# Kernel optimization log

Hardware: AMD Instinct MI355X
Metric: run time of the kernel (lower is better)

Reference implementation:

```python
import jax, jax.numpy as jnp
import numpy as np

B, S, D, H = 2, 2048, 1024, 16
HD = D // H  # 64


def setup_inputs() -> dict:
    key = jax.random.key(0)
    ks = jax.random.split(key, 5)
    sc = 1.0 / np.sqrt(D)
    return {
        "x": jax.random.normal(ks[0], (B, S, D), jnp.float32),
        "wq": jax.random.normal(ks[1], (D, D), jnp.float32) * sc,
        "bq": jnp.zeros((D,), jnp.float32),
        "wk": jax.random.normal(ks[2], (D, D), jnp.float32) * sc,
        "bk": jnp.zeros((D,), jnp.float32),
        "wv": jax.random.normal(ks[3], (D, D), jnp.float32) * sc,
        "bv": jnp.zeros((D,), jnp.float32),
        "wo": jax.random.normal(ks[4], (D, D), jnp.float32) * sc,
        "bo": jnp.zeros((D,), jnp.float32),
    }


def _rope_tables(seq_len, dim):
    inv_freq = 1.0 / (10000.0 ** (jnp.arange(0, dim, 2, dtype=jnp.float32) / dim))
    t = jnp.arange(seq_len, dtype=jnp.float32)
    freqs = jnp.einsum("i,j->ij", t, inv_freq)  # [S, dim/2]
    emb = jnp.concatenate([freqs, freqs], axis=-1)  # [S, dim]
    return jnp.cos(emb)[None, None], jnp.sin(emb)[None, None]  # [1,1,S,dim]


def _rotate_half(x):
    x1, x2 = x[..., : x.shape[-1] // 2], x[..., x.shape[-1] // 2 :]
    return jnp.concatenate([-x2, x1], axis=-1)


def reference(x, wq, bq, wk, bk, wv, bv, wo, bo):
    b, s, d = x.shape
    h, hd = H, d // H
    # projections (torch Linear: x @ W.T + b) -> [b, h, s, hd]
    def proj(w, bias):
        return (x @ w.T + bias).reshape(b, s, h, hd).transpose(0, 2, 1, 3)

    q, k, v = proj(wq, bq), proj(wk, bk), proj(wv, bv)
    cos, sin = _rope_tables(s, hd)
    q = q * cos + _rotate_half(q) * sin
    k = k * cos + _rotate_half(k) * sin
    scores = jnp.einsum("bhqd,bhkd->bhqk", q, k) / jnp.sqrt(jnp.float32(hd))
    attn = jax.nn.softmax(scores, axis=-1)
    out = jnp.einsum("bhqk,bhkd->bhqd", attn, v)
    out = out.transpose(0, 2, 1, 3).reshape(b, s, d)
    return out @ wo.T + bo
```

## Files before the change

kernel.cpp:

```cpp
#include <hip/hip_runtime.h>
#include <hip/hip_bf16.h>

#define Bq 2
#define Sq 2048
#define Dq 1024
#define Hq 16
#define QSCALE 0.18033688011112042f

typedef __attribute__((ext_vector_type(8))) short short8;
typedef __attribute__((ext_vector_type(4))) float floatx4;
typedef unsigned short ushort_t;

#define VMCNT0() asm volatile("s_waitcnt vmcnt(0)" ::: "memory")
#define GLDS(src, dst) __builtin_amdgcn_global_load_lds( \
    (const __attribute__((address_space(1))) void*)(src), \
    (__attribute__((address_space(3))) void*)(dst), 16, 0, 0)

__device__ __forceinline__ ushort_t f2bf(float f) {
    union { float f; unsigned u; } v; v.f = f;
    unsigned u = v.u;
    u += 0x7fffu + ((u >> 16) & 1u);
    return (ushort_t)(u >> 16);
}

__device__ __forceinline__ unsigned pk_bf16(float a, float b) {
    union { __hip_bfloat162 h; unsigned u; } c;
    c.h = __float22bfloat162_rn(float2{a, b});
    return c.u;
}

__device__ __forceinline__ void cvt8(const float* __restrict__ in, ushort_t* __restrict__ out, int i) {
    const float4* p = (const float4*)in + (size_t)i * 2;
    float4 a = p[0], b = p[1];
    ushort4 lo, hi;
    lo.x = f2bf(a.x); lo.y = f2bf(a.y); lo.z = f2bf(a.z); lo.w = f2bf(a.w);
    hi.x = f2bf(b.x); hi.y = f2bf(b.y); hi.z = f2bf(b.z); hi.w = f2bf(b.w);
    *(ushort4*)(out + (size_t)i * 8)     = lo;
    *(ushort4*)(out + (size_t)i * 8 + 4) = hi;
}

__global__ void prep(const float* __restrict__ x,
                     const float* __restrict__ wq, const float* __restrict__ wk,
                     const float* __restrict__ wv, const float* __restrict__ wo,
                     ushort_t* __restrict__ xb,
                     ushort_t* __restrict__ wqb, ushort_t* __restrict__ wkb,
                     ushort_t* __restrict__ wvb, ushort_t* __restrict__ wob,
                     float* __restrict__ cost, float* __restrict__ sint) {
    int b = blockIdx.x;
    if (b < 2048) {
        cvt8(x, xb, b * 256 + threadIdx.x);
    } else if (b < 4096) {
        int w = (b - 2048) >> 9;
        int i = ((b - 2048) & 511) * 256 + threadIdx.x;
        const float* src = (w == 0) ? wq : (w == 1) ? wk : (w == 2) ? wv : wo;
        ushort_t* dst    = (w == 0) ? wqb : (w == 1) ? wkb : (w == 2) ? wvb : wob;
        cvt8(src, dst, i);
    } else {
        int i = (b - 4096) * 256 + threadIdx.x;
        int s = i >> 5, f = i & 31;
        float invf = powf(10000.0f, -(float)f / 32.0f);
        float ang = (float)s * invf;
        cost[i] = cosf(ang);
        sint[i] = sinf(ang);
    }
}

__global__ __launch_bounds__(256, 3) void gemm_qkv(
    const ushort_t* __restrict__ xb,
    const ushort_t* __restrict__ wqb, const ushort_t* __restrict__ wkb, const ushort_t* __restrict__ wvb,
    const float* __restrict__ bq, const float* __restrict__ bk, const float* __restrict__ bv,
    const float* __restrict__ cost, const float* __restrict__ sint,
    ushort_t* __restrict__ qout, ushort_t* __restrict__ kout, ushort_t* __restrict__ vtout)
{
    __shared__ ushort_t As0[128 * 32], As1[128 * 32];
    __shared__ ushort_t Bs0[128 * 32], Bs1[128 * 32];
    const int mode = blockIdx.z;
    const ushort_t* W  = (mode == 0) ? wqb : (mode == 1) ? wkb : wvb;
    const float* bias  = (mode == 0) ? bq  : (mode == 1) ? bk  : bv;

    const int t = threadIdx.x;
    const int lane = t & 63;
    const int wid = t >> 6;
    const int l15 = lane & 15, lk = lane >> 4;
    const int wr = wid >> 1, wc = wid & 1;
    const int rowBase = blockIdx.y * 128;
    const int colBase = blockIdx.x * 128;

    floatx4 acc[4][4] = {};

    const char* aSrc[2];
    const char* bSrc[2];
    int ldso[2];
#pragma unroll
    for (int issue = 0; issue < 2; ++issue) {
        int ldsoff = issue * 4096 + t * 16;
        int row = ldsoff >> 6;
        int cb  = ldsoff & 63;
        ldso[issue] = ldsoff;
        aSrc[issue] = (const char*)xb + (size_t)(rowBase + row) * 2048 + cb;
        bSrc[issue] = (const char*)W  + (size_t)(colBase + row) * 2048 + cb;
    }

    auto STAGE = [&](ushort_t* Ad, ushort_t* Bd) {
#pragma unroll
        for (int issue = 0; issue < 2; ++issue) {
            GLDS(aSrc[issue], (char*)Ad + ldso[issue]);
            GLDS(bSrc[issue], (char*)Bd + ldso[issue]);
        }
        aSrc[0] += 64; aSrc[1] += 64; bSrc[0] += 64; bSrc[1] += 64;
    };

    auto KSTEP = [&](const ushort_t* Ac, const ushort_t* Bc, int knext, ushort_t* An, ushort_t* Bn) {
        if (knext < Dq) STAGE(An, Bn);
        short8 a[4], b[4];
#pragma unroll
        for (int m = 0; m < 4; ++m)
            a[m] = *(const short8*)((const char*)Ac + (wr * 64 + m * 16 + l15) * 64 + lk * 16);
#pragma unroll
        for (int n = 0; n < 4; ++n)
            b[n] = *(const short8*)((const char*)Bc + (wc * 64 + n * 16 + l15) * 64 + lk * 16);
        __builtin_amdgcn_s_setprio(1);
#pragma unroll
        for (int m = 0; m < 4; ++m)
#pragma unroll
            for (int n = 0; n < 4; ++n)
                acc[m][n] = __builtin_amdgcn_mfma_f32_16x16x32_bf16(a[m], b[n], acc[m][n], 0, 0, 0);
        __builtin_amdgcn_s_setprio(0);
        VMCNT0();
        __syncthreads();
    };

    STAGE(As0, Bs0);
    VMCNT0();
    __syncthreads();

#pragma unroll 1
    for (int k0 = 0; k0 < Dq; k0 += 64) {
        KSTEP(As0, Bs0, k0 + 32, As1, Bs1);
        KSTEP(As1, Bs1, k0 + 64, As0, Bs0);
    }

    const int colW = colBase + wc * 64;
    const int hh = colW >> 6;

    if (mode < 2) {
        ushort_t* outp = (mode == 0) ? qout : kout;
        const float osc = (mode == 0) ? QSCALE : 1.0f;
#pragma unroll
        for (int m = 0; m < 4; ++m) {
            int rg0 = rowBase + wr * 64 + m * 16 + lk * 4;
#pragma unroll
            for (int n2 = 0; n2 < 2; ++n2) {
                int d0 = n2 * 16 + l15;
                float b0 = bias[colW + d0];
                float b2 = bias[colW + d0 + 32];
#pragma unroll
                for (int r = 0; r < 4; ++r) {
                    int rg = rg0 + r;
                    int bb = rg >> 11;
                    int s  = rg & 2047;
                    float c  = cost[s * 32 + d0];
                    float sn = sint[s * 32 + d0];
                    float a0 = acc[m][n2][r]     + b0;
                    float a2 = acc[m][n2 + 2][r] + b2;
                    float o0 = (a0 * c - a2 * sn) * osc;
                    float o2 = (a2 * c + a0 * sn) * osc;
                    size_t base = ((size_t)(bb * Hq + hh) * Sq + s) * 64;
                    outp[base + d0]      = f2bf(o0);
                    outp[base + d0 + 32] = f2bf(o2);
                }
            }
        }
    } else {
#pragma unroll
        for (int m = 0; m < 4; ++m) {
            int rg0 = rowBase + wr * 64 + m * 16 + lk * 4;
            int bb  = rg0 >> 11;
            int s0  = rg0 & 2047;
            int g   = (s0 & 63) >> 2;
            int ng  = (g >> 3) * 8 + (g & 3) * 2 + ((g >> 2) & 1);
            int s2b = (s0 & ~63) + ng * 4;
#pragma unroll
            for (int n = 0; n < 4; ++n) {
                int d = n * 16 + l15;
                float bb_ = bias[colW + d];
#pragma unroll
                for (int r = 0; r < 4; ++r)
                    vtout[((size_t)(bb * Hq + hh) * 64 + d) * Sq + s2b + r] = f2bf(acc[m][n][r] + bb_);
            }
        }
    }
}

__global__ __launch_bounds__(256, 3) void flash_attn(
    const ushort_t* __restrict__ qbuf, const ushort_t* __restrict__ kbuf,
    const ushort_t* __restrict__ vtbuf, ushort_t* __restrict__ abuf)
{
    __shared__ char Ks0[64 * 128], Ks1[64 * 128];
    __shared__ char Vs0[64 * 128], Vs1[64 * 128];

    const int t = threadIdx.x, lane = t & 63, wid = t >> 6;
    const int l15 = lane & 15, lk = lane >> 4;

    int flat = blockIdx.y * 16 + blockIdx.x;
    flat = (flat & 7) * 64 + (flat >> 3);
    const int qtile = flat & 15, bh = flat >> 4;
    const int bpos = bh >> 4, h = bh & 15;
    const int qbase = qtile * 128 + wid * 32;

    const ushort_t* Qp = qbuf + ((size_t)bh * Sq + qbase) * 64;
    short8 qf[2][2];
#pragma unroll
    for (int mq = 0; mq < 2; ++mq)
#pragma unroll
        for (int kk = 0; kk < 2; ++kk)
            qf[mq][kk] = *(const short8*)(Qp + (mq * 16 + l15) * 64 + kk * 32 + lk * 8);

    short8 onesf;
#pragma unroll
    for (int j = 0; j < 8; ++j) onesf[j] = (short)0x3F80;

    floatx4 oacc[2][4] = {};
    floatx4 lacc[2] = {};

    int off_[4][2];
#pragma unroll
    for (int n = 0; n < 4; ++n) {
        int swz = (l15 & 7) << 4;
#pragma unroll
        for (int kk = 0; kk < 2; ++kk)
            off_[n][kk] = (n * 16 + l15) * 128 + ((kk * 64 + lk * 16) ^ swz);
    }

    const char* Kg = (const char*)kbuf  + (size_t)bh * Sq * 128;
    const char* Vg = (const char*)vtbuf + (size_t)bh * 64 * Sq * 2;
    unsigned kOff[2], vOff[2];
    int ldso[2];
#pragma unroll
    for (int issue = 0; issue < 2; ++issue) {
        int ldsoff = issue * 4096 + t * 16;
        int row = ldsoff >> 7;
        int pb  = ldsoff & 127;
        int lb  = pb ^ ((row & 7) << 4);
        ldso[issue] = ldsoff;
        kOff[issue] = (unsigned)(row * 128 + lb);
        vOff[issue] = (unsigned)(row * 4096 + lb);
    }

    auto STAGE = [&](char* Kd, char* Vd) {
#pragma unroll
        for (int issue = 0; issue < 2; ++issue) {
            GLDS(Kg + kOff[issue], Kd + ldso[issue]);
            GLDS(Vg + vOff[issue], Vd + ldso[issue]);
        }
        kOff[0] += 8192; kOff[1] += 8192; vOff[0] += 128; vOff[1] += 128;
    };

    auto TILE = [&](const char* Kc, const char* Vc, bool doStage, char* Kn, char* Vn) {
        if (doStage) STAGE(Kn, Vn);

        short8 kf[4][2];
#pragma unroll
        for (int n = 0; n < 4; ++n)
#pragma unroll
            for (int kk = 0; kk < 2; ++kk)
                kf[n][kk] = *(const short8*)(Kc + off_[n][kk]);

        floatx4 sacc[2][4] = {};
        __builtin_amdgcn_s_setprio(1);
#pragma unroll
        for (int kk = 0; kk < 2; ++kk)
#pragma unroll
            for (int n = 0; n < 4; ++n)
#pragma unroll
                for (int mq = 0; mq < 2; ++mq)
                    sacc[mq][n] = __builtin_amdgcn_mfma_f32_16x16x32_bf16(kf[n][kk], qf[mq][kk], sacc[mq][n], 0, 0, 0);
        __builtin_amdgcn_s_setprio(0);

        short8 vf[4][2];
#pragma unroll
        for (int n = 0; n < 4; ++n)
#pragma unroll
            for (int kb = 0; kb < 2; ++kb)
                vf[n][kb] = *(const short8*)(Vc + off_[n][kb]);

        short8 paf[2][2];
#pragma unroll
        for (int mq = 0; mq < 2; ++mq) {
            float p[4][4];
#pragma unroll
            for (int n = 0; n < 4; ++n)
#pragma unroll
                for (int r = 0; r < 4; ++r)
                    p[n][r] = __builtin_exp2f(sacc[mq][n][r]);
#pragma unroll
            for (int kb = 0; kb < 2; ++kb) {
                union { unsigned u[4]; short8 v; } pu;
                pu.u[0] = pk_bf16(p[2 * kb][0],     p[2 * kb][1]);
                pu.u[1] = pk_bf16(p[2 * kb][2],     p[2 * kb][3]);
                pu.u[2] = pk_bf16(p[2 * kb + 1][0], p[2 * kb + 1][1]);
                pu.u[3] = pk_bf16(p[2 * kb + 1][2], p[2 * kb + 1][3]);
                paf[mq][kb] = pu.v;
            }
        }

        __builtin_amdgcn_s_setprio(1);
#pragma unroll
        for (int kb = 0; kb < 2; ++kb) {
#pragma unroll
            for (int n = 0; n < 4; ++n)
#pragma unroll
                for (int mq = 0; mq < 2; ++mq)
                    oacc[mq][n] = __builtin_amdgcn_mfma_f32_16x16x32_bf16(paf[mq][kb], vf[n][kb], oacc[mq][n], 0, 0, 0);
#pragma unroll
            for (int mq = 0; mq < 2; ++mq)
                lacc[mq] = __builtin_amdgcn_mfma_f32_16x16x32_bf16(paf[mq][kb], onesf, lacc[mq], 0, 0, 0);
        }
        __builtin_amdgcn_s_setprio(0);

        VMCNT0();
        __syncthreads();
    };

    STAGE(Ks0, Vs0);
    VMCNT0();
    __syncthreads();

#pragma unroll 1
    for (int i = 0; i < 15; ++i) {
        TILE(Ks0, Vs0, true, Ks1, Vs1);
        TILE(Ks1, Vs1, true, Ks0, Vs0);
    }
    TILE(Ks0, Vs0, true,  Ks1, Vs1);
    TILE(Ks1, Vs1, false, Ks0, Vs0);

#pragma unroll
    for (int mq = 0; mq < 2; ++mq)
#pragma unroll
        for (int r = 0; r < 4; ++r) {
            float linv = 1.0f / lacc[mq][r];
            int srow = qbase + mq * 16 + lk * 4 + r;
            size_t base = ((size_t)bpos * Sq + srow) * Dq + h * 64;
#pragma unroll
            for (int n = 0; n < 4; ++n)
                abuf[base + n * 16 + l15] = f2bf(oacc[mq][n][r] * linv);
        }
}

__global__ __launch_bounds__(256, 4) void gemm_out(
    const ushort_t* __restrict__ ab, const ushort_t* __restrict__ wob,
    const float* __restrict__ bo, float* __restrict__ out)
{
    __shared__ ushort_t As0[128 * 32], As1[128 * 32];
    __shared__ ushort_t Bs0[64 * 32],  Bs1[64 * 32];
    const int t = threadIdx.x;
    const int lane = t & 63;
    const int wid = t >> 6;
    const int l15 = lane & 15, lk = lane >> 4;
    const int wr = wid >> 1, wc = wid & 1;
    const int rowBase = blockIdx.y * 128;
    const int colBase = blockIdx.x * 64;

    floatx4 acc[4][2] = {};

    const char* aSrc[2];
    const char* bSrc;
    int ldso[2];
#pragma unroll
    for (int issue = 0; issue < 2; ++issue) {
        int ldsoff = issue * 4096 + t * 16;
        int row = ldsoff >> 6;
        int cb  = ldsoff & 63;
        ldso[issue] = ldsoff;
        aSrc[issue] = (const char*)ab + (size_t)(rowBase + row) * 2048 + cb;
    }
    {
        int ldsoff = t * 16;
        int row = ldsoff >> 6;
        int cb  = ldsoff & 63;
        bSrc = (const char*)wob + (size_t)(colBase + row) * 2048 + cb;
    }

    auto STAGE = [&](ushort_t* Ad, ushort_t* Bd) {
#pragma unroll
        for (int issue = 0; issue < 2; ++issue)
            GLDS(aSrc[issue], (char*)Ad + ldso[issue]);
        GLDS(bSrc, (char*)Bd + ldso[0]);
        aSrc[0] += 64; aSrc[1] += 64; bSrc += 64;
    };

    auto KSTEP = [&](const ushort_t* Ac, const ushort_t* Bc, int knext, ushort_t* An, ushort_t* Bn) {
        if (knext < Dq) STAGE(An, Bn);
        short8 a[4], b[2];
#pragma unroll
        for (int m = 0; m < 4; ++m)
            a[m] = *(const short8*)((const char*)Ac + (wr * 64 + m * 16 + l15) * 64 + lk * 16);
#pragma unroll
        for (int n = 0; n < 2; ++n)
            b[n] = *(const short8*)((const char*)Bc + (wc * 32 + n * 16 + l15) * 64 + lk * 16);
        __builtin_amdgcn_s_setprio(1);
#pragma unroll
        for (int m = 0; m < 4; ++m)
#pragma unroll
            for (int n = 0; n < 2; ++n)
                acc[m][n] = __builtin_amdgcn_mfma_f32_16x16x32_bf16(a[m], b[n], acc[m][n], 0, 0, 0);
        __builtin_amdgcn_s_setprio(0);
        VMCNT0();
        __syncthreads();
    };

    STAGE(As0, Bs0);
    VMCNT0();
    __syncthreads();

#pragma unroll 1
    for (int k0 = 0; k0 < Dq; k0 += 64) {
        KSTEP(As0, Bs0, k0 + 32, As1, Bs1);
        KSTEP(As1, Bs1, k0 + 64, As0, Bs0);
    }

    const int colW = colBase + wc * 32;
#pragma unroll
    for (int m = 0; m < 4; ++m) {
        int rg0 = rowBase + wr * 64 + m * 16 + lk * 4;
#pragma unroll
        for (int n = 0; n < 2; ++n) {
            int colg = colW + n * 16 + l15;
            float bb_ = bo[colg];
#pragma unroll
            for (int r = 0; r < 4; ++r)
                out[(size_t)(rg0 + r) * Dq + colg] = acc[m][n][r] + bb_;
        }
    }
}

extern "C" void kernel_launch(void* const* d_in, const int* in_sizes, int n_in,
                              void* d_out, int out_size, void* d_ws, size_t ws_size,
                              hipStream_t stream) {
    (void)in_sizes; (void)n_in; (void)out_size;
    const float* x  = (const float*)d_in[0];
    const float* wq = (const float*)d_in[1];
    const float* bq = (const float*)d_in[2];
    const float* wk = (const float*)d_in[3];
    const float* bk = (const float*)d_in[4];
    const float* wv = (const float*)d_in[5];
    const float* bv = (const float*)d_in[6];
    const float* wo = (const float*)d_in[7];
    const float* bo = (const float*)d_in[8];
    float* out = (float*)d_out;

    if (ws_size < 50855936) return;
    char* ws = (char*)d_ws;
    ushort_t* xb   = (ushort_t*)(ws + 0);
    ushort_t* wqb  = (ushort_t*)(ws + 8388608);
    ushort_t* wkb  = (ushort_t*)(ws + 10485760);
    ushort_t* wvb  = (ushort_t*)(ws + 12582912);
    ushort_t* wob  = (ushort_t*)(ws + 14680064);
    ushort_t* qb   = (ushort_t*)(ws + 16777216);
    ushort_t* kb   = (ushort_t*)(ws + 25165824);
    ushort_t* vtb  = (ushort_t*)(ws + 33554432);
    ushort_t* abuf = (ushort_t*)(ws + 41943040);
    float*    cost = (float*)(ws + 50331648);
    float*    sint = (float*)(ws + 50593792);

    prep<<<4352, 256, 0, stream>>>(x, wq, wk, wv, wo, xb, wqb, wkb, wvb, wob, cost, sint);
    gemm_qkv<<<dim3(8, 32, 3), 256, 0, stream>>>(xb, wqb, wkb, wvb, bq, bk, bv, cost, sint, qb, kb, vtb);
    flash_attn<<<dim3(16, 32), 256, 0, stream>>>(qb, kb, vtb, abuf);
    gemm_out<<<dim3(16, 32), 256, 0, stream>>>(abuf, wob, bo, out);
}
```

Measured before the change: 118.9 us.

## Triple-buffer K/V tiles in flash attention with partial vmcnt waits

Moves the flash attention K/V staging from double to triple buffering in LDS. Two tiles are kept in flight, and each step waits only for the older load (vmcnt(4)) before the barrier instead of draining all loads, so global-to-LDS latency can overlap more compute. The cost is 16KB more LDS per block, which may reduce occupancy below the launch bound of 3 blocks per CU. It also adds a more complex loop schedule, with 30 steps in the main loop plus 2 tail tiles.

Result: no change. 119.3 us (+0.3%).

```diff
diff --git a/kernel.cpp b/kernel.cpp
--- a/kernel.cpp
+++ b/kernel.cpp
@@ -196,8 +196,8 @@
     const ushort_t* __restrict__ qbuf, const ushort_t* __restrict__ kbuf,
     const ushort_t* __restrict__ vtbuf, ushort_t* __restrict__ abuf)
 {
-    __shared__ char Ks0[64 * 128], Ks1[64 * 128];
-    __shared__ char Vs0[64 * 128], Vs1[64 * 128];
+    __shared__ char Ks0[64 * 128], Ks1[64 * 128], Ks2[64 * 128];
+    __shared__ char Vs0[64 * 128], Vs1[64 * 128], Vs2[64 * 128];
 
     const int t = threadIdx.x, lane = t & 63, wid = t >> 6;
     const int l15 = lane & 15, lk = lane >> 4;
@@ -256,7 +256,20 @@
         kOff[0] += 8192; kOff[1] += 8192; vOff[0] += 128; vOff[1] += 128;
     };
 
-    auto TILE = [&](const char* Kc, const char* Vc, bool doStage, char* Kn, char* Vn) {
+    auto BAR4 = [&]() {
+        asm volatile("s_waitcnt vmcnt(4)" ::: "memory");
+        __builtin_amdgcn_s_barrier();
+        asm volatile("" ::: "memory");
+        __builtin_amdgcn_sched_barrier(0);
+    };
+    auto BAR0 = [&]() {
+        asm volatile("s_waitcnt vmcnt(0)" ::: "memory");
+        __builtin_amdgcn_s_barrier();
+        asm volatile("" ::: "memory");
+        __builtin_amdgcn_sched_barrier(0);
+    };
+
+    auto TILE = [&](const char* Kc, const char* Vc, char* Kn, char* Vn, bool doStage, bool deep) {
         if (doStage) STAGE(Kn, Vn);
 
         short8 kf[4][2];
@@ -318,21 +331,21 @@
         }
         __builtin_amdgcn_s_setprio(0);
 
-        VMCNT0();
-        __syncthreads();
+        if (deep) BAR4(); else BAR0();
     };
 
     STAGE(Ks0, Vs0);
-    VMCNT0();
-    __syncthreads();
+    STAGE(Ks1, Vs1);
+    BAR4();
 
 #pragma unroll 1
-    for (int i = 0; i < 15; ++i) {
-        TILE(Ks0, Vs0, true, Ks1, Vs1);
-        TILE(Ks1, Vs1, true, Ks0, Vs0);
-    }
-    TILE(Ks0, Vs0, true,  Ks1, Vs1);
-    TILE(Ks1, Vs1, false, Ks0, Vs0);
+    for (int i = 0; i < 10; ++i) {
+        TILE(Ks0, Vs0, Ks2, Vs2, true, true);
+        TILE(Ks1, Vs1, Ks0, Vs0, true, true);
+        TILE(Ks2, Vs2, Ks1, Vs1, true, true);
+    }
+    TILE(Ks0, Vs0, Ks0, Vs0, false, false);
+    TILE(Ks1, Vs1, Ks0, Vs0, false, false);
 
 #pragma unroll
     for (int mq = 0; mq < 2; ++mq)
```

## Double KV tile per barrier in attention and widen out-proj K-step with swizzle

Applied to the files above, without the earlier changes.

The flash attention kernel now stages 128 keys per double-buffered stage and processes them as two 64-key sub-tiles, which halves the number of barrier/vmcnt waits over the sequence. The output GEMM doubles its K-step to 64 elements, switches to 128-byte LDS rows with an XOR swizzle, and halves the number of synchronisation points. LDS use doubles in both kernels, and gemm_out's occupancy hint drops from 4 to 3, which may reduce latency hiding.

Measured after the change: 119.4 us. Within noise of the previous version (+0.4%).

```diff
diff --git a/kernel.cpp b/kernel.cpp
--- a/kernel.cpp
+++ b/kernel.cpp
@@ -196,8 +196,8 @@
     const ushort_t* __restrict__ qbuf, const ushort_t* __restrict__ kbuf,
     const ushort_t* __restrict__ vtbuf, ushort_t* __restrict__ abuf)
 {
-    __shared__ char Ks0[64 * 128], Ks1[64 * 128];
-    __shared__ char Vs0[64 * 128], Vs1[64 * 128];
+    __shared__ char Ks0[16384], Ks1[16384];
+    __shared__ char Vs0[16384], Vs1[16384];
 
     const int t = threadIdx.x, lane = t & 63, wid = t >> 6;
     const int l15 = lane & 15, lk = lane >> 4;
@@ -250,73 +250,81 @@
     auto STAGE = [&](char* Kd, char* Vd) {
 #pragma unroll
         for (int issue = 0; issue < 2; ++issue) {
-            GLDS(Kg + kOff[issue], Kd + ldso[issue]);
-            GLDS(Vg + vOff[issue], Vd + ldso[issue]);
-        }
-        kOff[0] += 8192; kOff[1] += 8192; vOff[0] += 128; vOff[1] += 128;
+            GLDS(Kg + kOff[issue],        Kd + ldso[issue]);
+            GLDS(Kg + kOff[issue] + 8192, Kd + 8192 + ldso[issue]);
+            GLDS(Vg + vOff[issue],        Vd + ldso[issue]);
+            GLDS(Vg + vOff[issue] + 128,  Vd + 8192 + ldso[issue]);
+        }
+        kOff[0] += 16384; kOff[1] += 16384; vOff[0] += 256; vOff[1] += 256;
     };
 
     auto TILE = [&](const char* Kc, const char* Vc, bool doStage, char* Kn, char* Vn) {
         if (doStage) STAGE(Kn, Vn);
 
-        short8 kf[4][2];
-#pragma unroll
-        for (int n = 0; n < 4; ++n)
+#pragma unroll
+        for (int sub = 0; sub < 2; ++sub) {
+            const char* Kcs = Kc + sub * 8192;
+            const char* Vcs = Vc + sub * 8192;
+
+            short8 kf[4][2];
+#pragma unroll
+            for (int n = 0; n < 4; ++n)
+#pragma unroll
+                for (int kk = 0; kk < 2; ++kk)
+                    kf[n][kk] = *(const short8*)(Kcs + off_[n][kk]);
+
+            floatx4 sacc[2][4] = {};
+            __builtin_amdgcn_s_setprio(1);
 #pragma unroll
             for (int kk = 0; kk < 2; ++kk)
-                kf[n][kk] = *(const short8*)(Kc + off_[n][kk]);
-
-        floatx4 sacc[2][4] = {};
-        __builtin_amdgcn_s_setprio(1);
-#pragma unroll
-        for (int kk = 0; kk < 2; ++kk)
+#pragma unroll
+                for (int n = 0; n < 4; ++n)
+#pragma unroll
+                    for (int mq = 0; mq < 2; ++mq)
+                        sacc[mq][n] = __builtin_amdgcn_mfma_f32_16x16x32_bf16(kf[n][kk], qf[mq][kk], sacc[mq][n], 0, 0, 0);
+            __builtin_amdgcn_s_setprio(0);
+
+            short8 vf[4][2];
 #pragma unroll
             for (int n = 0; n < 4; ++n)
 #pragma unroll
+                for (int kb = 0; kb < 2; ++kb)
+                    vf[n][kb] = *(const short8*)(Vcs + off_[n][kb]);
+
+            short8 paf[2][2];
+#pragma unroll
+            for (int mq = 0; mq < 2; ++mq) {
+                float p[4][4];
+#pragma unroll
+                for (int n = 0; n < 4; ++n)
+#pragma unroll
+                    for (int r = 0; r < 4; ++r)
+                        p[n][r] = __builtin_exp2f(sacc[mq][n][r]);
+#pragma unroll
+                for (int kb = 0; kb < 2; ++kb) {
+                    union { unsigned u[4]; short8 v; } pu;
+                    pu.u[0] = pk_bf16(p[2 * kb][0],     p[2 * kb][1]);
+                    pu.u[1] = pk_bf16(p[2 * kb][2],     p[2 * kb][3]);
+                    pu.u[2] = pk_bf16(p[2 * kb + 1][0], p[2 * kb + 1][1]);
+                    pu.u[3] = pk_bf16(p[2 * kb + 1][2], p[2 * kb + 1][3]);
+                    paf[mq][kb] = pu.v;
+                }
+            }
+
+            __builtin_amdgcn_s_setprio(1);
+#pragma unroll
+            for (int kb = 0; kb < 2; ++kb) {
+#pragma unroll
+                for (int n = 0; n < 4; ++n)
+#pragma unroll
+                    for (int mq = 0; mq < 2; ++mq)
+                        oacc[mq][n] = __builtin_amdgcn_mfma_f32_16x16x32_bf16(paf[mq][kb], vf[n][kb], oacc[mq][n], 0, 0, 0);
+#pragma unroll
                 for (int mq = 0; mq < 2; ++mq)
-                    sacc[mq][n] = __builtin_amdgcn_mfma_f32_16x16x32_bf16(kf[n][kk], qf[mq][kk], sacc[mq][n], 0, 0, 0);
-        __builtin_amdgcn_s_setprio(0);
-
-        short8 vf[4][2];
-#pragma unroll
-        for (int n = 0; n < 4; ++n)
-#pragma unroll
-            for (int kb = 0; kb < 2; ++kb)
-                vf[n][kb] = *(const short8*)(Vc + off_[n][kb]);
-
-        short8 paf[2][2];
-#pragma unroll
-        for (int mq = 0; mq < 2; ++mq) {
-            float p[4][4];
-#pragma unroll
-            for (int n = 0; n < 4; ++n)
-#pragma unroll
-                for (int r = 0; r < 4; ++r)
-                    p[n][r] = __builtin_exp2f(sacc[mq][n][r]);
-#pragma unroll
-            for (int kb = 0; kb < 2; ++kb) {
-                union { unsigned u[4]; short8 v; } pu;
-                pu.u[0] = pk_bf16(p[2 * kb][0],     p[2 * kb][1]);
-                pu.u[1] = pk_bf16(p[2 * kb][2],     p[2 * kb][3]);
-                pu.u[2] = pk_bf16(p[2 * kb + 1][0], p[2 * kb + 1][1]);
-                pu.u[3] = pk_bf16(p[2 * kb + 1][2], p[2 * kb + 1][3]);
-                paf[mq][kb] = pu.v;
+                    lacc[mq] = __builtin_amdgcn_mfma_f32_16x16x32_bf16(paf[mq][kb], onesf, lacc[mq], 0, 0, 0);
             }
-        }
-
-        __builtin_amdgcn_s_setprio(1);
-#pragma unroll
-        for (int kb = 0; kb < 2; ++kb) {
-#pragma unroll
-            for (int n = 0; n < 4; ++n)
-#pragma unroll
-                for (int mq = 0; mq < 2; ++mq)
-                    oacc[mq][n] = __builtin_amdgcn_mfma_f32_16x16x32_bf16(paf[mq][kb], vf[n][kb], oacc[mq][n], 0, 0, 0);
-#pragma unroll
-            for (int mq = 0; mq < 2; ++mq)
-                lacc[mq] = __builtin_amdgcn_mfma_f32_16x16x32_bf16(paf[mq][kb], onesf, lacc[mq], 0, 0, 0);
-        }
-        __builtin_amdgcn_s_setprio(0);
+            __builtin_amdgcn_s_setprio(0);
+        }
 
         VMCNT0();
         __syncthreads();
@@ -327,7 +335,7 @@
     __syncthreads();
 
 #pragma unroll 1
-    for (int i = 0; i < 15; ++i) {
+    for (int i = 0; i < 7; ++i) {
         TILE(Ks0, Vs0, true, Ks1, Vs1);
         TILE(Ks1, Vs1, true, Ks0, Vs0);
     }
@@ -347,12 +355,12 @@
         }
 }
 
-__global__ __launch_bounds__(256, 4) void gemm_out(
+__global__ __launch_bounds__(256, 3) void gemm_out(
     const ushort_t* __restrict__ ab, const ushort_t* __restrict__ wob,
     const float* __restrict__ bo, float* __restrict__ out)
 {
-    __shared__ ushort_t As0[128 * 32], As1[128 * 32];
-    __shared__ ushort_t Bs0[64 * 32],  Bs1[64 * 32];
+    __shared__ ushort_t As0[128 * 64], As1[128 * 64];
+    __shared__ ushort_t Bs0[64 * 64],  Bs1[64 * 64];
     const int t = threadIdx.x;
     const int lane = t & 63;
     const int wid = t >> 6;
@@ -363,47 +371,74 @@
 
     floatx4 acc[4][2] = {};
 
-    const char* aSrc[2];
-    const char* bSrc;
-    int ldso[2];
+    const int swz = (l15 & 7) << 4;
+    int aoff_[4][2], boff_[2][2];
+#pragma unroll
+    for (int m = 0; m < 4; ++m)
+#pragma unroll
+        for (int kk = 0; kk < 2; ++kk)
+            aoff_[m][kk] = (wr * 64 + m * 16 + l15) * 128 + ((kk * 64 + lk * 16) ^ swz);
+#pragma unroll
+    for (int n = 0; n < 2; ++n)
+#pragma unroll
+        for (int kk = 0; kk < 2; ++kk)
+            boff_[n][kk] = (wc * 32 + n * 16 + l15) * 128 + ((kk * 64 + lk * 16) ^ swz);
+
+    const char* aSrc[4];
+    const char* bSrc[2];
+    int ldsoA[4], ldsoB[2];
+#pragma unroll
+    for (int issue = 0; issue < 4; ++issue) {
+        int ldsoff = issue * 4096 + t * 16;
+        int row = ldsoff >> 7;
+        int pb  = ldsoff & 127;
+        int lb  = pb ^ ((row & 7) << 4);
+        ldsoA[issue] = ldsoff;
+        aSrc[issue] = (const char*)ab + (size_t)(rowBase + row) * 2048 + lb;
+    }
 #pragma unroll
     for (int issue = 0; issue < 2; ++issue) {
         int ldsoff = issue * 4096 + t * 16;
-        int row = ldsoff >> 6;
-        int cb  = ldsoff & 63;
-        ldso[issue] = ldsoff;
-        aSrc[issue] = (const char*)ab + (size_t)(rowBase + row) * 2048 + cb;
-    }
-    {
-        int ldsoff = t * 16;
-        int row = ldsoff >> 6;
-        int cb  = ldsoff & 63;
-        bSrc = (const char*)wob + (size_t)(colBase + row) * 2048 + cb;
+        int row = ldsoff >> 7;
+        int pb  = ldsoff & 127;
+        int lb  = pb ^ ((row & 7) << 4);
+        ldsoB[issue] = ldsoff;
+        bSrc[issue] = (const char*)wob + (size_t)(colBase + row) * 2048 + lb;
     }
 
     auto STAGE = [&](ushort_t* Ad, ushort_t* Bd) {
 #pragma unroll
+        for (int issue = 0; issue < 4; ++issue)
+            GLDS(aSrc[issue], (char*)Ad + ldsoA[issue]);
+#pragma unroll
         for (int issue = 0; issue < 2; ++issue)
-            GLDS(aSrc[issue], (char*)Ad + ldso[issue]);
-        GLDS(bSrc, (char*)Bd + ldso[0]);
-        aSrc[0] += 64; aSrc[1] += 64; bSrc += 64;
+            GLDS(bSrc[issue], (char*)Bd + ldsoB[issue]);
+#pragma unroll
+        for (int issue = 0; issue < 4; ++issue) aSrc[issue] += 128;
+        bSrc[0] += 128; bSrc[1] += 128;
     };
 
     auto KSTEP = [&](const ushort_t* Ac, const ushort_t* Bc, int knext, ushort_t* An, ushort_t* Bn) {
         if (knext < Dq) STAGE(An, Bn);
-        short8 a[4], b[2];
+        short8 a[4][2], b[2][2];
 #pragma unroll
         for (int m = 0; m < 4; ++m)
-            a[m] = *(const short8*)((const char*)Ac + (wr * 64 + m * 16 + l15) * 64 + lk * 16);
+#pragma unroll
+            for (int kk = 0; kk < 2; ++kk)
+                a[m][kk] = *(const short8*)((const char*)Ac + aoff_[m][kk]);
 #pragma unroll
         for (int n = 0; n < 2; ++n)
-            b[n] = *(const short8*)((const char*)Bc + (wc * 32 + n * 16 + l15) * 64 + lk * 16);
+#pragma unroll
+            for (int kk = 0; kk < 2; ++kk)
+                b[n][kk] = *(const short8*)((const char*)Bc + boff_[n][kk]);
         __builtin_amdgcn_s_setprio(1);
 #pragma unroll
-        for (int m = 0; m < 4; ++m)
-#pragma unroll
-            for (int n = 0; n < 2; ++n)
-                acc[m][n] = __builtin_amdgcn_mfma_f32_16x16x32_bf16(a[m], b[n], acc[m][n], 0, 0, 0);
+        for (int kk = 0; kk < 2; ++kk)
+#pragma unroll
+            for (int m = 0; m < 4; ++m)
+#pragma unroll
+                for (int n = 0; n < 2; ++n)
+                    acc[m][n] = __builtin_amdgcn_mfma_f32_16x16x32_bf16(a[m][kk], b[n][kk], acc[m][n], 0, 0, 0);
         __builtin_amdgcn_s_setprio(0);
         VMCNT0();
         __syncthreads();
@@ -414,9 +449,9 @@
     __syncthreads();
 
 #pragma unroll 1
-    for (int k0 = 0; k0 < Dq; k0 += 64) {
-        KSTEP(As0, Bs0, k0 + 32, As1, Bs1);
-        KSTEP(As1, Bs1, k0 + 64, As0, Bs0);
+    for (int k0 = 0; k0 < Dq; k0 += 128) {
+        KSTEP(As0, Bs0, k0 + 64,  As1, Bs1);
+        KSTEP(As1, Bs1, k0 + 128, As0, Bs0);
     }
 
     const int colW = colBase + wc * 32;
```
